# Optimization experiments

Hardware: AMD Instinct MI355X
Metric: run time of the kernel (lower is better)

The kernel has to match this reference:

```python
import jax, jax.numpy as jnp
import numpy as np

B, S, D = 2, 2048, 1024
E, K = 8, 2
H = 1792  # round_up(int(1024*5/3)=1706, 256)


def setup_inputs() -> dict:
    key = jax.random.key(0)
    k1, k2, k3, k4, k5 = jax.random.split(key, 5)
    scale = 0.02
    x = jax.random.normal(k1, (B, S, D), dtype=jnp.float32)
    gate_w = jax.random.normal(k2, (E, D), dtype=jnp.float32) * scale   # nn.Linear(D,E).weight
    w_gate = jax.random.normal(k3, (E, D, H), dtype=jnp.float32) * scale
    w_up = jax.random.normal(k4, (E, D, H), dtype=jnp.float32) * scale
    w_down = jax.random.normal(k5, (E, H, D), dtype=jnp.float32) * scale
    return {"x": x, "gate_w": gate_w, "w_gate": w_gate, "w_up": w_up, "w_down": w_down}


def reference(x, gate_w, w_gate, w_up, w_down):
    b, s, d = x.shape
    x_flat = x.reshape(-1, d)                      # [T, D]
    # Gate computed in bf16 (torch autocast) then cast back to f32.
    logits = (x_flat.astype(jnp.bfloat16) @ gate_w.T.astype(jnp.bfloat16)).astype(jnp.float32)  # [T, E]
    topk_w, topk_idx = jax.lax.top_k(logits, K)    # [T, K]
    topk_w = jax.nn.softmax(topk_w, axis=-1)
    probs = jax.nn.softmax(logits, axis=-1)        # [T, E]
    mean_probs = probs.mean(0)                     # [E]
    load_balance_loss = E * jnp.sum(mean_probs ** 2)
    # Per-token combine weight for each expert (equivalent to sort/split/index_add combine).
    combine = jnp.sum(jax.nn.one_hot(topk_idx, E, dtype=x_flat.dtype) * topk_w[..., None], axis=1)  # [T, E]
    out = jnp.zeros_like(x_flat)
    for e in range(E):  # fixed small expert loop; math identical to grouped dispatch
        g = x_flat @ w_gate[e]                     # [T, H]
        u = x_flat @ w_up[e]                       # [T, H]
        y = (jax.nn.silu(g) * u) @ w_down[e]       # [T, D]
        out = out + y * combine[:, e:e + 1]
    return out.reshape(b, s, d), load_balance_loss, mean_probs
```

## Files before the change

### kernel.cpp

```cpp
#include <hip/hip_runtime.h>
#include <stdint.h>

#define TT 4096
#define DD 1024
#define EE 8
#define HH 1792
#define MP 10240
#define MT128 80

typedef __attribute__((ext_vector_type(8))) short short8;
typedef __attribute__((ext_vector_type(4))) short short4v;
typedef __attribute__((ext_vector_type(4))) float f32x4;

static __device__ __forceinline__ unsigned short f2bf(float f) {
  union { float f; uint32_t u; } v; v.f = f;
  return (unsigned short)((v.u + 0x7fffu + ((v.u >> 16) & 1u)) >> 16);
}
static __device__ __forceinline__ float bf2f(unsigned short h) {
  union { uint32_t u; float f; } v; v.u = ((uint32_t)h) << 16;
  return v.f;
}

static __device__ __forceinline__ void gll16(const void* g, const void* l) {
  __builtin_amdgcn_global_load_lds(
      (const __attribute__((address_space(1))) unsigned int*)g,
      (__attribute__((address_space(3))) unsigned int*)l, 16, 0, 0);
}

__global__ __launch_bounds__(256) void prep_gate(
    const float* __restrict__ w_gate, const float* __restrict__ w_up,
    const float* __restrict__ w_down, unsigned short* __restrict__ wguT,
    unsigned short* __restrict__ wdT,
    const float* __restrict__ x, const float* __restrict__ gw,
    float2* __restrict__ wts, float* __restrict__ probs, int2* __restrict__ topk,
    unsigned short* __restrict__ xbf) {
  __shared__ float L0[64][65];
  const int tid = threadIdx.x;
  const int lr = tid >> 2, lc = (tid & 3) * 16;
  int bid = blockIdx.x;
  if (bid < 10752) {
    const int kind = bid / 3584;
    const int rr = bid % 3584;
    const int e = rr / 448, r = rr % 448;
    if (kind < 2) {
      const int bx = r / 28, by = r % 28;
      const float* src = (kind == 0 ? w_gate : w_up) +
                         (size_t)e * DD * HH + (size_t)(bx * 64) * HH + by * 64;
#pragma unroll
      for (int q = 0; q < 4; ++q) {
        const f32x4 v = *(const f32x4*)(src + (size_t)lr * HH + lc + 4 * q);
#pragma unroll
        for (int j = 0; j < 4; ++j) L0[lr][lc + 4 * q + j] = v[j];
      }
      __syncthreads();
      unsigned short b0[16];
#pragma unroll
      for (int q = 0; q < 16; ++q) b0[q] = f2bf(L0[lc + q][lr]);
      const int h = by * 64 + lr;
      const int pg = (h >> 4) * 32 + kind * 16 + (h & 15);
      unsigned short* dst = wguT + (size_t)e * 2 * HH * DD + (size_t)pg * DD +
                            (size_t)bx * 64 + lc;
      *(short8*)(dst) = *(const short8*)&b0[0];
      *(short8*)(dst + 8) = *(const short8*)&b0[8];
    } else {
      const int bx = r / 16, by = r % 16;
      const float* src = w_down + (size_t)e * HH * DD + (size_t)(bx * 64) * DD + by * 64;
#pragma unroll
      for (int q = 0; q < 4; ++q) {
        const f32x4 v = *(const f32x4*)(src + (size_t)lr * DD + lc + 4 * q);
#pragma unroll
        for (int j = 0; j < 4; ++j) L0[lr][lc + 4 * q + j] = v[j];
      }
      __syncthreads();
      unsigned short b0[16];
#pragma unroll
      for (int q = 0; q < 16; ++q) b0[q] = f2bf(L0[lc + q][lr]);
      const int d = by * 64 + lr;
      unsigned short* dst = wdT + (size_t)e * DD * HH + (size_t)d * HH + bx * 64 + lc;
      *(short8*)(dst) = *(const short8*)&b0[0];
      *(short8*)(dst + 8) = *(const short8*)&b0[8];
    }
  } else {
    const int lane = tid & 63;
    const int wave = tid >> 6;
    const int t = (bid - 10752) * 4 + wave;
    const float* xr = x + (size_t)t * DD;
    float acc[EE];
#pragma unroll
    for (int e = 0; e < EE; ++e) acc[e] = 0.f;
#pragma unroll
    for (int i = 0; i < DD / 256; ++i) {
      const int d = (i * 64 + lane) * 4;
      const f32x4 xv = *(const f32x4*)(xr + d);
      unsigned short us[4];
      float xb[4];
#pragma unroll
      for (int j = 0; j < 4; ++j) { us[j] = f2bf(xv[j]); xb[j] = bf2f(us[j]); }
      *(short4v*)(xbf + (size_t)t * DD + d) = *(const short4v*)us;
#pragma unroll
      for (int e = 0; e < EE; ++e) {
        const f32x4 gv = *(const f32x4*)(gw + e * DD + d);
#pragma unroll
        for (int j = 0; j < 4; ++j) acc[e] += xb[j] * bf2f(f2bf(gv[j]));
      }
    }
#pragma unroll
    for (int e = 0; e < EE; ++e) {
#pragma unroll
      for (int off = 32; off > 0; off >>= 1)
        acc[e] += __shfl_xor(acc[e], off, 64);
    }
    if (lane == 0) {
      float lg[EE];
#pragma unroll
      for (int e = 0; e < EE; ++e) lg[e] = bf2f(f2bf(acc[e]));
      float m1 = -1e30f, m2 = -1e30f; int i1 = 0, i2 = 0;
#pragma unroll
      for (int e = 0; e < EE; ++e) {
        const float v = lg[e];
        if (v > m1) { m2 = m1; i2 = i1; m1 = v; i1 = e; }
        else if (v > m2) { m2 = v; i2 = e; }
      }
      const float e2 = expf(m2 - m1);
      const float w1 = 1.f / (1.f + e2);
      float p[EE]; float s = 0.f;
#pragma unroll
      for (int e = 0; e < EE; ++e) { p[e] = expf(lg[e] - m1); s += p[e]; }
      const float inv = 1.f / s;
#pragma unroll
      for (int e = 0; e < EE; ++e) probs[(size_t)t * EE + e] = p[e] * inv;
      wts[t] = make_float2(w1, e2 * w1);
      topk[t] = make_int2(i1, i2);
    }
  }
}

__global__ __launch_bounds__(512) void route_kernel(
    const int2* __restrict__ topk, const float2* __restrict__ wts,
    const float* __restrict__ probs, int* __restrict__ tok_list,
    float* __restrict__ wt_list, int* __restrict__ tab128, float* __restrict__ tail) {
  const int lane = threadIdx.x & 63;
  const int e = threadIdx.x >> 6;
  __shared__ int cnts[EE], offs[EE];
  __shared__ float sm[EE];
  int cnt = 0;
  for (int i = 0; i < TT / 64; ++i) {
    const int2 k2 = topk[i * 64 + lane];
    cnt += __popcll(__ballot(k2.x == e || k2.y == e));
  }
  if (lane == 0) cnts[e] = cnt;
  __syncthreads();
  if (threadIdx.x == 0) {
    int off = 0, n128 = 0;
    for (int f = 0; f < EE; ++f) {
      offs[f] = off;
      const int pc = (cnts[f] + 127) & ~127;
      for (int j = 0; j < (pc >> 7); ++j) {
        tab128[2 * n128] = f; tab128[2 * n128 + 1] = off + 128 * j; ++n128;
      }
      off += pc;
    }
    for (; n128 < MT128; ++n128) { tab128[2 * n128] = -1; tab128[2 * n128 + 1] = 0; }
  }
  __syncthreads();
  int pos = offs[e];
  for (int i = 0; i < TT / 64; ++i) {
    const int t = i * 64 + lane;
    const int2 k2 = topk[t];
    const bool sel = (k2.x == e || k2.y == e);
    const unsigned long long m = __ballot(sel);
    if (sel) {
      const int p = pos + __popcll(m & ((1ull << lane) - 1ull));
      const float2 w2v = wts[t];
      tok_list[p] = t;
      wt_list[p] = (k2.x == e) ? w2v.x : -w2v.y;
    }
    pos += __popcll(m);
  }
  const int pc = (cnt + 127) & ~127;
  for (int s = cnt + lane; s < pc; s += 64) {
    tok_list[offs[e] + s] = 0;
    wt_list[offs[e] + s] = 0.f;
  }
  float racc = 0.f;
  for (int t = lane; t < TT; t += 64) racc += probs[(size_t)t * EE + e];
#pragma unroll
  for (int off = 32; off > 0; off >>= 1) racc += __shfl_xor(racc, off, 64);
  if (lane == 0) {
    const float m = racc * (1.f / TT);
    sm[e] = m;
    tail[1 + e] = m;
  }
  __syncthreads();
  if (threadIdx.x == 0) {
    float loss = 0.f;
#pragma unroll
    for (int f = 0; f < EE; ++f) loss += sm[f] * sm[f];
    tail[0] = (float)EE * loss;
  }
}

template <int MODE>
static __device__ __forceinline__ void gemm_body(
    const unsigned short* __restrict__ Ab, const unsigned short* __restrict__ Bb,
    const int* __restrict__ tab, const int* __restrict__ tok_list,
    const float* __restrict__ wt_list, unsigned short* __restrict__ dst) {
  constexpr int K   = (MODE == 0) ? DD : HH;
  constexpr int NBR = (MODE == 0) ? 2 * HH : DD;
  constexpr int NNT = NBR / 128;
  __shared__ unsigned short As[128 * 64];
  __shared__ unsigned short Bs[128 * 64];

  const int nwg = gridDim.x;
  const int wgid = (blockIdx.x & 7) * (nwg >> 3) + (blockIdx.x >> 3);
  int mt, nt;
  if constexpr (MODE == 1) { mt = wgid % MT128; nt = wgid / MT128; }
  else                     { mt = wgid / NNT;   nt = wgid % NNT; }
  const int e = tab[2 * mt];
  if (e < 0) return;
  const int row0 = tab[2 * mt + 1];
  const int n0 = nt * 128;

  const int tid = threadIdx.x, lane = tid & 63, wave = tid >> 6;
  const int wm = (wave >> 1) * 64, wn = (wave & 1) * 64;
  const int fr = lane & 15, hi = lane >> 4;

  const unsigned short* Bt = Bb + ((size_t)e * NBR + n0) * K;

  const int srel = tid * 16;
  const int srow0 = srel >> 7;
  const int sch = (srel >> 4) & 7;

  const unsigned short* srcA[4];
#pragma unroll
  for (int q = 0; q < 4; ++q) {
    const int row = q * 32 + srow0;
    const int swz = (sch ^ (row & 7)) << 3;
    if constexpr (MODE == 0)
      srcA[q] = Ab + (size_t)tok_list[row0 + row] * DD + swz;
    else
      srcA[q] = Ab + (size_t)(row0 + row) * K + swz;
  }

  f32x4 acc[4][4];
#pragma unroll
  for (int i = 0; i < 4; ++i)
#pragma unroll
    for (int j = 0; j < 4; ++j) acc[i][j] = (f32x4){0.f, 0.f, 0.f, 0.f};

  for (int k0 = 0; k0 < K; k0 += 64) {
#pragma unroll
    for (int q = 0; q < 4; ++q)
      gll16(srcA[q] + k0, (const char*)As + q * 4096 + srel);
#pragma unroll
    for (int q = 0; q < 4; ++q) {
      const int row = q * 32 + srow0;
      gll16(Bt + (size_t)row * K + k0 + ((sch ^ (row & 7)) << 3),
            (const char*)Bs + q * 4096 + srel);
    }
    __syncthreads();
#pragma unroll
    for (int kc = 0; kc < 2; ++kc) {
      short8 a[4], b[4];
#pragma unroll
      for (int i = 0; i < 4; ++i) {
        const int row = wm + i * 16 + fr;
        a[i] = *(const short8*)((const char*)As + ((row * 128 + kc * 64 + hi * 16) ^ ((row & 7) << 4)));
      }
#pragma unroll
      for (int j = 0; j < 4; ++j) {
        const int row = wn + j * 16 + fr;
        b[j] = *(const short8*)((const char*)Bs + ((row * 128 + kc * 64 + hi * 16) ^ ((row & 7) << 4)));
      }
#pragma unroll
      for (int i = 0; i < 4; ++i)
#pragma unroll
        for (int j = 0; j < 4; ++j)
          acc[i][j] = __builtin_amdgcn_mfma_f32_16x16x32_bf16(a[i], b[j], acc[i][j], 0, 0, 0);
    }
    __syncthreads();
  }

  const int r4 = hi * 4;
  if constexpr (MODE == 0) {
#pragma unroll
    for (int i = 0; i < 4; ++i)
#pragma unroll
      for (int r = 0; r < 4; ++r) {
        const int row = row0 + wm + i * 16 + r4 + r;
#pragma unroll
        for (int jj = 0; jj < 2; ++jj) {
          const float g = acc[i][2 * jj][r], u = acc[i][2 * jj + 1][r];
          const int nb = n0 + wn + jj * 32;
          const int h = ((nb >> 5) << 4) + fr;
          dst[(size_t)row * HH + h] = f2bf((g / (1.f + expf(-g))) * u);
        }
      }
  } else {
#pragma unroll
    for (int i = 0; i < 4; ++i)
#pragma unroll
      for (int r = 0; r < 4; ++r) {
        const int rl = row0 + wm + i * 16 + r4 + r;
        const int tok = tok_list[rl];
        const float ws = wt_list[rl];
        if (ws != 0.f) {
          const int slot = (ws < 0.f) ? 1 : 0;
          const float wt = fabsf(ws);
          unsigned short* prow = dst + (size_t)slot * TT * DD + (size_t)tok * DD;
#pragma unroll
          for (int j = 0; j < 4; ++j)
            prow[n0 + wn + j * 16 + fr] = f2bf(acc[i][j][r] * wt);
        }
      }
  }
}

__global__ __launch_bounds__(256, 3) void gemm_gu(
    const unsigned short* __restrict__ Ab, const unsigned short* __restrict__ Bb,
    const int* __restrict__ tab, const int* __restrict__ tok_list,
    unsigned short* __restrict__ act) {
  gemm_body<0>(Ab, Bb, tab, tok_list, nullptr, act);
}

__global__ __launch_bounds__(256, 3) void gemm_dn(
    const unsigned short* __restrict__ Ab, const unsigned short* __restrict__ Bb,
    const int* __restrict__ tab, const int* __restrict__ tok_list,
    const float* __restrict__ wt_list, unsigned short* __restrict__ part) {
  gemm_body<1>(Ab, Bb, tab, tok_list, wt_list, part);
}

__global__ __launch_bounds__(256) void combine_kernel(
    const unsigned short* __restrict__ part, float* __restrict__ out) {
  const size_t i = ((size_t)blockIdx.x * 256 + threadIdx.x) * 8;
  const short8 p0 = *(const short8*)(part + i);
  const short8 p1 = *(const short8*)(part + (size_t)TT * DD + i);
  f32x4 o0, o1;
#pragma unroll
  for (int j = 0; j < 4; ++j) {
    o0[j] = bf2f((unsigned short)p0[j]) + bf2f((unsigned short)p1[j]);
    o1[j] = bf2f((unsigned short)p0[4 + j]) + bf2f((unsigned short)p1[4 + j]);
  }
  *(f32x4*)(out + i) = o0;
  *(f32x4*)(out + i + 4) = o1;
}

extern "C" void kernel_launch(void* const* d_in, const int* in_sizes, int n_in,
                              void* d_out, int out_size, void* d_ws, size_t ws_size,
                              hipStream_t stream) {
  const float* x      = (const float*)d_in[0];
  const float* gw     = (const float*)d_in[1];
  const float* w_gate = (const float*)d_in[2];
  const float* w_up   = (const float*)d_in[3];
  const float* w_down = (const float*)d_in[4];
  float* out = (float*)d_out;
  float* tail = out + (size_t)TT * DD;

  char* w = (char*)d_ws;
  size_t o = 0;
  auto carve = [&](size_t bytes) { char* p = w + o; o += (bytes + 255) & ~255ull; return p; };
  unsigned short* wguT = (unsigned short*)carve((size_t)EE * 2 * HH * DD * 2);
  unsigned short* wdT  = (unsigned short*)carve((size_t)EE * DD * HH * 2);
  unsigned short* xbf  = (unsigned short*)carve((size_t)TT * DD * 2);
  unsigned short* act  = (unsigned short*)carve((size_t)MP * HH * 2);
  float2* wts    = (float2*)carve((size_t)TT * 8);
  float* probs   = (float*)carve((size_t)TT * EE * 4);
  int2* topk     = (int2*)carve((size_t)TT * 8);
  int* tok_list  = (int*)carve((size_t)MP * 4);
  float* wt_list = (float*)carve((size_t)MP * 4);
  int* tab128    = (int*)carve((size_t)MT128 * 8);
  unsigned short* part = wguT;

  prep_gate<<<11776, 256, 0, stream>>>(w_gate, w_up, w_down, wguT, wdT,
                                       x, gw, wts, probs, topk, xbf);
  route_kernel<<<1, 512, 0, stream>>>(topk, wts, probs, tok_list, wt_list, tab128, tail);

  gemm_gu<<<MT128 * 28, 256, 0, stream>>>(xbf, wguT, tab128, tok_list, act);
  gemm_dn<<<MT128 * 8, 256, 0, stream>>>(act, wdT, tab128, tok_list, wt_list, part);
  combine_kernel<<<TT * DD / 2048, 256, 0, stream>>>(part, out);
}
```

Before: 262.8 us.

## Overlap w_down bf16 transpose with gate/up GEMM in one launch

Moves the w_down fp32-to-bf16 transpose out of the prep kernel and appends its tiles as extra blocks in the gate/up GEMM grid. The memory-bound conversion can then run alongside the compute-bound GEMM instead of serially before it. Shared memory is now a single buffer reused by both paths. The extra blocks sit at the end of the grid and compete with GEMM blocks for bandwidth and occupancy.

```diff
diff --git a/kernel.cpp b/kernel.cpp
--- a/kernel.cpp
+++ b/kernel.cpp
@@ -7,6 +7,7 @@
 #define HH 1792
 #define MP 10240
 #define MT128 80
+#define GU_GRID (MT128 * 28)
 
 typedef __attribute__((ext_vector_type(8))) short short8;
 typedef __attribute__((ext_vector_type(4))) short short4v;
@@ -27,63 +28,70 @@
       (__attribute__((address_space(3))) unsigned int*)l, 16, 0, 0);
 }
 
-__global__ __launch_bounds__(256) void prep_gate(
+static __device__ __forceinline__ void prep_gu_tile(
+    float (*L0)[65], int kind, int rr, const float* __restrict__ w_gate,
+    const float* __restrict__ w_up, unsigned short* __restrict__ wguT, int tid) {
+  const int lr = tid >> 2, lc = (tid & 3) * 16;
+  const int e = rr / 448, r = rr % 448;
+  const int bx = r / 28, by = r % 28;
+  const float* src = (kind == 0 ? w_gate : w_up) +
+                     (size_t)e * DD * HH + (size_t)(bx * 64 + lr) * HH + by * 64;
+#pragma unroll
+  for (int q = 0; q < 4; ++q) {
+    const f32x4 v = *(const f32x4*)(src + lc + 4 * q);
+#pragma unroll
+    for (int j = 0; j < 4; ++j) L0[lr][lc + 4 * q + j] = v[j];
+  }
+  __syncthreads();
+  unsigned short b0[16];
+#pragma unroll
+  for (int q = 0; q < 16; ++q) b0[q] = f2bf(L0[lc + q][lr]);
+  const int h = by * 64 + lr;
+  const int pg = (h >> 4) * 32 + kind * 16 + (h & 15);
+  unsigned short* dst = wguT + (size_t)e * 2 * HH * DD + (size_t)pg * DD +
+                        (size_t)bx * 64 + lc;
+  *(short8*)(dst) = *(const short8*)&b0[0];
+  *(short8*)(dst + 8) = *(const short8*)&b0[8];
+}
+
+static __device__ __forceinline__ void prep_dn_tile(
+    float (*L0)[65], int rr, const float* __restrict__ w_down,
+    unsigned short* __restrict__ wdT, int tid) {
+  const int lr = tid >> 2, lc = (tid & 3) * 16;
+  const int e = rr / 448, r = rr % 448;
+  const int bx = r / 16, by = r % 16;
+  const float* src = w_down + (size_t)e * HH * DD + (size_t)(bx * 64 + lr) * DD + by * 64;
+#pragma unroll
+  for (int q = 0; q < 4; ++q) {
+    const f32x4 v = *(const f32x4*)(src + lc + 4 * q);
+#pragma unroll
+    for (int j = 0; j < 4; ++j) L0[lr][lc + 4 * q + j] = v[j];
+  }
+  __syncthreads();
+  unsigned short b0[16];
+#pragma unroll
+  for (int q = 0; q < 16; ++q) b0[q] = f2bf(L0[lc + q][lr]);
+  const int d = by * 64 + lr;
+  unsigned short* dst = wdT + (size_t)e * DD * HH + (size_t)d * HH + bx * 64 + lc;
+  *(short8*)(dst) = *(const short8*)&b0[0];
+  *(short8*)(dst + 8) = *(const short8*)&b0[8];
+}
+
+__global__ __launch_bounds__(256) void prep_gu_gate(
     const float* __restrict__ w_gate, const float* __restrict__ w_up,
-    const float* __restrict__ w_down, unsigned short* __restrict__ wguT,
-    unsigned short* __restrict__ wdT,
+    unsigned short* __restrict__ wguT,
     const float* __restrict__ x, const float* __restrict__ gw,
     float2* __restrict__ wts, float* __restrict__ probs, int2* __restrict__ topk,
     unsigned short* __restrict__ xbf) {
   __shared__ float L0[64][65];
   const int tid = threadIdx.x;
-  const int lr = tid >> 2, lc = (tid & 3) * 16;
-  int bid = blockIdx.x;
-  if (bid < 10752) {
-    const int kind = bid / 3584;
-    const int rr = bid % 3584;
-    const int e = rr / 448, r = rr % 448;
-    if (kind < 2) {
-      const int bx = r / 28, by = r % 28;
-      const float* src = (kind == 0 ? w_gate : w_up) +
-                         (size_t)e * DD * HH + (size_t)(bx * 64) * HH + by * 64;
-#pragma unroll
-      for (int q = 0; q < 4; ++q) {
-        const f32x4 v = *(const f32x4*)(src + (size_t)lr * HH + lc + 4 * q);
-#pragma unroll
-        for (int j = 0; j < 4; ++j) L0[lr][lc + 4 * q + j] = v[j];
-      }
-      __syncthreads();
-      unsigned short b0[16];
-#pragma unroll
-      for (int q = 0; q < 16; ++q) b0[q] = f2bf(L0[lc + q][lr]);
-      const int h = by * 64 + lr;
-      const int pg = (h >> 4) * 32 + kind * 16 + (h & 15);
-      unsigned short* dst = wguT + (size_t)e * 2 * HH * DD + (size_t)pg * DD +
-                            (size_t)bx * 64 + lc;
-      *(short8*)(dst) = *(const short8*)&b0[0];
-      *(short8*)(dst + 8) = *(const short8*)&b0[8];
-    } else {
-      const int bx = r / 16, by = r % 16;
-      const float* src = w_down + (size_t)e * HH * DD + (size_t)(bx * 64) * DD + by * 64;
-#pragma unroll
-      for (int q = 0; q < 4; ++q) {
-        const f32x4 v = *(const f32x4*)(src + (size_t)lr * DD + lc + 4 * q);
-#pragma unroll
-        for (int j = 0; j < 4; ++j) L0[lr][lc + 4 * q + j] = v[j];
-      }
-      __syncthreads();
-      unsigned short b0[16];
-#pragma unroll
-      for (int q = 0; q < 16; ++q) b0[q] = f2bf(L0[lc + q][lr]);
-      const int d = by * 64 + lr;
-      unsigned short* dst = wdT + (size_t)e * DD * HH + (size_t)d * HH + bx * 64 + lc;
-      *(short8*)(dst) = *(const short8*)&b0[0];
-      *(short8*)(dst + 8) = *(const short8*)&b0[8];
-    }
+  const int bid = blockIdx.x;
+  if (bid < 7168) {
+    prep_gu_tile(L0, bid / 3584, bid % 3584, w_gate, w_up, wguT, tid);
   } else {
     const int lane = tid & 63;
     const int wave = tid >> 6;
-    const int t = (bid - 10752) * 4 + wave;
+    const int t = (bid - 7168) * 4 + wave;
     const float* xr = x + (size_t)t * DD;
     float acc[EE];
 #pragma unroll
@@ -202,17 +210,15 @@
 
 template <int MODE>
 static __device__ __forceinline__ void gemm_body(
+    unsigned short* As, unsigned short* Bs, int bid, int nwg,
     const unsigned short* __restrict__ Ab, const unsigned short* __restrict__ Bb,
     const int* __restrict__ tab, const int* __restrict__ tok_list,
     const float* __restrict__ wt_list, unsigned short* __restrict__ dst) {
   constexpr int K   = (MODE == 0) ? DD : HH;
   constexpr int NBR = (MODE == 0) ? 2 * HH : DD;
   constexpr int NNT = NBR / 128;
-  __shared__ unsigned short As[128 * 64];
-  __shared__ unsigned short Bs[128 * 64];
-
-  const int nwg = gridDim.x;
-  const int wgid = (blockIdx.x & 7) * (nwg >> 3) + (blockIdx.x >> 3);
+
+  const int wgid = (bid & 7) * (nwg >> 3) + (bid >> 3);
   int mt, nt;
   if constexpr (MODE == 1) { mt = wgid % MT128; nt = wgid / MT128; }
   else                     { mt = wgid / NNT;   nt = wgid % NNT; }
@@ -316,18 +322,28 @@
   }
 }
 
-__global__ __launch_bounds__(256, 3) void gemm_gu(
+__global__ __launch_bounds__(256, 3) void gemm_gu_pd(
     const unsigned short* __restrict__ Ab, const unsigned short* __restrict__ Bb,
     const int* __restrict__ tab, const int* __restrict__ tok_list,
-    unsigned short* __restrict__ act) {
-  gemm_body<0>(Ab, Bb, tab, tok_list, nullptr, act);
+    unsigned short* __restrict__ act,
+    const float* __restrict__ w_down, unsigned short* __restrict__ wdT) {
+  __shared__ char smem[32768] __attribute__((aligned(16)));
+  const int bid = blockIdx.x;
+  if (bid < GU_GRID) {
+    gemm_body<0>((unsigned short*)smem, (unsigned short*)(smem + 16384),
+                 bid, GU_GRID, Ab, Bb, tab, tok_list, nullptr, act);
+  } else {
+    prep_dn_tile((float(*)[65])smem, bid - GU_GRID, w_down, wdT, threadIdx.x);
+  }
 }
 
 __global__ __launch_bounds__(256, 3) void gemm_dn(
     const unsigned short* __restrict__ Ab, const unsigned short* __restrict__ Bb,
     const int* __restrict__ tab, const int* __restrict__ tok_list,
     const float* __restrict__ wt_list, unsigned short* __restrict__ part) {
-  gemm_body<1>(Ab, Bb, tab, tok_list, wt_list, part);
+  __shared__ char smem[32768] __attribute__((aligned(16)));
+  gemm_body<1>((unsigned short*)smem, (unsigned short*)(smem + 16384),
+               blockIdx.x, gridDim.x, Ab, Bb, tab, tok_list, wt_list, part);
 }
 
 __global__ __launch_bounds__(256) void combine_kernel(
@@ -371,11 +387,11 @@
   int* tab128    = (int*)carve((size_t)MT128 * 8);
   unsigned short* part = wguT;
 
-  prep_gate<<<11776, 256, 0, stream>>>(w_gate, w_up, w_down, wguT, wdT,
-                                       x, gw, wts, probs, topk, xbf);
+  prep_gu_gate<<<8192, 256, 0, stream>>>(w_gate, w_up, wguT, x, gw, wts, probs, topk, xbf);
   route_kernel<<<1, 512, 0, stream>>>(topk, wts, probs, tok_list, wt_list, tab128, tail);
 
-  gemm_gu<<<MT128 * 28, 256, 0, stream>>>(xbf, wguT, tab128, tok_list, act);
+  gemm_gu_pd<<<GU_GRID + 3584, 256, 0, stream>>>(xbf, wguT, tab128, tok_list, act,
+                                                 w_down, wdT);
   gemm_dn<<<MT128 * 8, 256, 0, stream>>>(act, wdT, tab128, tok_list, wt_list, part);
   combine_kernel<<<TT * DD / 2048, 256, 0, stream>>>(part, out);
 }
```

After: 256.7 us. 1.02x faster.
